# Optimization experiments

Hardware: AMD Instinct MI355X
Metric: run time of the kernel (lower is better)

The kernel has to match this reference:

```python
import jax, jax.numpy as jnp
import numpy as np

B, N, M, K = 4, 16384, 16384, 16   # batch, points, centers, neighbors
C, O, G = 64, 64, 8                # in_planes, out_planes, group


def setup_inputs() -> dict:
    key = jax.random.key(0)
    ks = jax.random.split(key, 16)
    r = lambda i, sh, s=1.0: jax.random.normal(ks[i], sh, jnp.float32) * s
    return dict(
        center_pos=r(0, (B, M, 3)),
        center_fea=r(1, (B, C, M)),
        pos=r(2, (B, N, 3)),
        fea=r(3, (B, C, N)),
        idx=jax.random.randint(ks[4], (B, M, K), 0, N, jnp.int32),
        # linear q/k/v
        Wq=r(5, (C, O), 0.05), bq=jnp.zeros((O,), jnp.float32),
        Wk=r(6, (C, O), 0.05), bk=jnp.zeros((O,), jnp.float32),
        Wv=r(7, (C, O), 0.05), bv=jnp.zeros((O,), jnp.float32),
        # center_pos_encode: conv1x1(3->O, no bias) + folded BN (scale,shift) + relu + conv1x1(O->O)
        cpe_w1=r(8, (3, O), 0.05), cpe_s=jnp.ones((O,), jnp.float32), cpe_b=jnp.zeros((O,), jnp.float32),
        cpe_w2=r(9, (O, O), 0.05), cpe_b2=jnp.zeros((O,), jnp.float32),
        # pos_encode (Conv2d 1x1 == per-point linear)
        pe_w1=r(10, (3, O), 0.05), pe_s=jnp.ones((O,), jnp.float32), pe_b=jnp.zeros((O,), jnp.float32),
        pe_w2=r(11, (O, O), 0.05), pe_b2=jnp.zeros((O,), jnp.float32),
        # weight_encode (O -> G)
        we_w1=r(12, (O, G), 0.05), we_s=jnp.ones((G,), jnp.float32), we_b=jnp.zeros((G,), jnp.float32),
        we_w2=r(13, (G, G), 0.05), we_b2=jnp.zeros((G,), jnp.float32),
    )


def _mlp2(x, w1, s, b, w2, b2):
    # conv1x1(no bias) -> inference BatchNorm folded to (scale, shift) -> ReLU -> conv1x1(+bias)
    h = jax.nn.relu(x @ w1 * s + b)
    return h @ w2 + b2


def reference(center_pos, center_fea, pos, fea, idx,
              Wq, bq, Wk, bk, Wv, bv,
              cpe_w1, cpe_s, cpe_b, cpe_w2, cpe_b2,
              pe_w1, pe_s, pe_b, pe_w2, pe_b2,
              we_w1, we_s, we_b, we_w2, we_b2):
    x_q = center_fea.transpose(0, 2, 1) @ Wq + bq        # [B,M,O]
    ft = fea.transpose(0, 2, 1)                          # [B,N,C]
    x_k = ft @ Wk + bk                                   # [B,N,O]
    x_v = ft @ Wv + bv                                   # [B,N,O]

    gather = jax.vmap(lambda a, i: a[i])                 # per-batch irregular gather
    nk = gather(x_k, idx)                                # [B,M,K,O]
    nv = gather(x_v, idx)                                # [B,M,K,O]
    npos = gather(pos, idx) - center_pos[:, :, None, :]  # [B,M,K,3] relative coords

    cpr = _mlp2(center_pos, cpe_w1, cpe_s, cpe_b, cpe_w2, cpe_b2)  # [B,M,O]
    pr = _mlp2(npos, pe_w1, pe_s, pe_b, pe_w2, pe_b2)              # [B,M,K,O]

    r_qk = nk - x_q[:, :, None, :] + cpr[:, :, None, :]  # [B,M,K,O]
    v = nv + pr                                          # [B,M,K,O]

    w = _mlp2(r_qk, we_w1, we_s, we_b, we_w2, we_b2)     # [B,M,K,G]
    w = jax.nn.softmax(w, axis=2)                        # softmax over neighbors

    v = v.reshape(B, M, K, G, O // G)
    out = jnp.einsum('bmkgi,bmkg->bmgi', v, w).reshape(B, M, O)
    return out.transpose(0, 2, 1)                        # [B,O,M]
```

## Files before the change

### kernel.cpp

```cpp
#include <hip/hip_runtime.h>
#include <hip/hip_bf16.h>

typedef unsigned short u16;
typedef __attribute__((ext_vector_type(8))) __bf16 bf8v;
typedef __attribute__((ext_vector_type(8))) _Float16 f16x8;
typedef __attribute__((ext_vector_type(2))) _Float16 h2v;
typedef __attribute__((ext_vector_type(4))) float f32x4;
typedef __attribute__((ext_vector_type(4))) unsigned uint4v;

#define B_ 4
#define N_ 16384
#define M_ 16384
#define K_ 16
#define C_ 64
#define O_ 64
#define G_ 8

__device__ __forceinline__ float bf2f(u16 x){
  union { unsigned u; float f; } v; v.u = ((unsigned)x) << 16; return v.f;
}
__device__ __forceinline__ u16 f2bf(float f){
  union { float f; unsigned u; } v; v.f = f;
  unsigned u = v.u;
  return (u16)((u + 0x7FFFu + ((u >> 16) & 1u)) >> 16);
}
__device__ __forceinline__ u16 f2h(float f){
  union { _Float16 h; u16 u; } v; v.h = (_Float16)f; return v.u;
}
__device__ __forceinline__ h2v mkh2(float a, float b){
  h2v r = {(_Float16)a, (_Float16)b}; return r;
}

__global__ __launch_bounds__(256) void pre_kernel(
    const float* __restrict__ center_pos, const float* __restrict__ center_fea,
    const float* __restrict__ pos, const float* __restrict__ fea,
    const float* __restrict__ Wq, const float* __restrict__ bq,
    const float* __restrict__ Wk, const float* __restrict__ bk,
    const float* __restrict__ Wv, const float* __restrict__ bv,
    const float* __restrict__ cpe_w1, const float* __restrict__ cpe_s, const float* __restrict__ cpe_b,
    const float* __restrict__ cpe_w2, const float* __restrict__ cpe_b2,
    const float* __restrict__ we_w1,
    u16* __restrict__ xk, u16* __restrict__ xv, float* __restrict__ qw,
    float* __restrict__ pos4, float* __restrict__ cp4)
{
  __shared__ u16 sWT[128*72];
  __shared__ u16 sA[64*72];
  __shared__ u16 sOut[64*136];
  __shared__ float sMisc[256];
  __shared__ float sCi[8];
  int tid = threadIdx.x;
  int l = tid & 63, w = tid >> 6, c = l & 15, q = l >> 4;
  int blk = blockIdx.x;

  if (blk < 256){
    int P0 = blk * 256; int b = P0 >> 14; int n00 = P0 & (N_-1);
    const float* fb = fea + (long)b*C_*N_;
    for (int e = tid; e < 8192; e += 256){
      int k = e >> 7, col = e & 127;
      float v = (col < 64) ? Wk[k*64 + col] : Wv[k*64 + (col-64)];
      sWT[col*72 + k] = f2bf(v);
    }
    if (tid < 128) sMisc[tid] = (tid < 64) ? bk[tid] : bv[tid-64];
    {
      long pg = (long)P0 + tid;
      f32x4 r = {pos[pg*3], pos[pg*3+1], pos[pg*3+2], 0.f};
      ((f32x4*)pos4)[pg] = r;
    }

    #pragma unroll 1
    for (int s = 0; s < 4; s++){
      int n0 = n00 + s*64;
      #pragma unroll
      for (int pp = 0; pp < 4; pp++){
        int k = pp*16 + (tid >> 4);
        int nf = (tid & 15)*4;
        f32x4 v = *(const f32x4*)&fb[(long)k*N_ + n0 + nf];
        sA[(nf+0)*72+k] = f2bf(v[0]); sA[(nf+1)*72+k] = f2bf(v[1]);
        sA[(nf+2)*72+k] = f2bf(v[2]); sA[(nf+3)*72+k] = f2bf(v[3]);
      }
      __syncthreads();

      bf8v af0 = *(const bf8v*)&sA[(w*16+c)*72 + q*8];
      bf8v af1 = *(const bf8v*)&sA[(w*16+c)*72 + 32 + q*8];
      f32x4 acc[8];
      #pragma unroll
      for (int t = 0; t < 8; t++){
        float bb = sMisc[16*t + c];
        f32x4 a_ = {bb, bb, bb, bb};
        bf8v b0 = *(const bf8v*)&sWT[(16*t + c)*72 + q*8];
        bf8v b1 = *(const bf8v*)&sWT[(16*t + c)*72 + 32 + q*8];
        a_ = __builtin_amdgcn_mfma_f32_16x16x32_bf16(af0, b0, a_, 0,0,0);
        a_ = __builtin_amdgcn_mfma_f32_16x16x32_bf16(af1, b1, a_, 0,0,0);
        acc[t] = a_;
      }
      #pragma unroll
      for (int t = 0; t < 8; t++)
        #pragma unroll
        for (int r = 0; r < 4; r++)
          sOut[(w*16 + q*4 + r)*136 + 16*t + c] = f2bf(acc[t][r]);
      __syncthreads();

      #pragma unroll
      for (int rep = 0; rep < 4; rep++){
        int chunk = rep*256 + tid;
        int pt = chunk >> 4, c8i = chunk & 15;
        uint4v val = *(const uint4v*)&sOut[pt*136 + c8i*8];
        int col8 = c8i*8;
        long row = (long)P0 + s*64 + pt;
        if (col8 < 64) *(uint4v*)(xk + row*64 + col8)      = val;
        else           *(uint4v*)(xv + row*64 + (col8-64)) = val;
      }
      __syncthreads();
    }
  } else {
    int P0 = (blk - 256) * 256; int b = P0 >> 14; int m00 = P0 & (M_-1);
    const float* cfb = center_fea + (long)b*C_*M_;
    float* sWe = (float*)sOut;
    float* sQ  = (float*)sOut;
    for (int e = tid; e < 512; e += 256) sWe[e] = we_w1[e];
    if (tid < 64){
      float sc = cpe_s[tid];
      sMisc[tid]     = cpe_w1[tid]*sc;
      sMisc[64+tid]  = cpe_w1[64+tid]*sc;
      sMisc[128+tid] = cpe_w1[128+tid]*sc;
      sMisc[192+tid] = cpe_b[tid];
    }
    {
      long pg = (long)P0 + tid;
      f32x4 r = {center_pos[pg*3], center_pos[pg*3+1], center_pos[pg*3+2], 0.f};
      ((f32x4*)cp4)[pg] = r;
    }
    __syncthreads();
    {
      int k = tid >> 1, g0 = (tid & 1)*4;
      const float* brow = (k < 64) ? (cpe_w2 + k*64) : (Wq + (k-64)*64);
      float sgn = (k < 64) ? 1.f : -1.f;
      float aw[4] = {0.f,0.f,0.f,0.f};
      for (int o = 0; o < 64; o++){
        float bo = brow[o]*sgn;
        #pragma unroll
        for (int gg=0; gg<4; gg++) aw[gg] += bo * sWe[o*8 + g0+gg];
      }
      #pragma unroll
      for (int gg=0; gg<4; gg++) sWT[(g0+gg)*136 + k] = f2bf(aw[gg]);
    }
    for (int e = tid; e < 2176; e += 256){
      int r = e / 136, cc = e % 136;
      if (r >= 8 || cc >= 128) sWT[e] = 0;
    }
    if (tid < 8){
      float s = 0.f;
      for (int o = 0; o < 64; o++) s += (cpe_b2[o] - bq[o]) * sWe[o*8 + tid];
      sCi[tid] = s;
    }
    __syncthreads();

    #pragma unroll 1
    for (int s = 0; s < 4; s++){
      int m0 = m00 + s*64;
      #pragma unroll
      for (int pp = 0; pp < 4; pp++){
        int k = pp*16 + (tid >> 4);
        int nf = (tid & 15)*4;
        f32x4 v = *(const f32x4*)&cfb[(long)k*M_ + m0 + nf];
        sA[(nf+0)*72+k] = f2bf(v[0]); sA[(nf+1)*72+k] = f2bf(v[1]);
        sA[(nf+2)*72+k] = f2bf(v[2]); sA[(nf+3)*72+k] = f2bf(v[3]);
      }
      long c3 = (long)(P0 + s*64 + w*16 + c)*3;
      float cp0 = center_pos[c3], cp1 = center_pos[c3+1], cp2 = center_pos[c3+2];
      __syncthreads();

      bf8v ah[2];
      #pragma unroll
      for (int ks = 0; ks < 2; ks++){
        union { bf8v v; u16 sv[8]; } ua;
        #pragma unroll
        for (int j = 0; j < 8; j++){
          int h = ks*32 + q*8 + j;
          float hv = cp0*sMisc[h] + cp1*sMisc[64+h] + cp2*sMisc[128+h] + sMisc[192+h];
          ua.sv[j] = f2bf(fmaxf(hv, 0.f));
        }
        ah[ks] = ua.v;
      }
      bf8v acf0 = *(const bf8v*)&sA[(w*16+c)*72 + q*8];
      bf8v acf1 = *(const bf8v*)&sA[(w*16+c)*72 + 32 + q*8];

      float ci = (c < 8) ? sCi[c] : 0.f;
      f32x4 aq = {ci, ci, ci, ci};
      {
        bf8v b0 = *(const bf8v*)&sWT[c*136 + q*8];
        bf8v b1 = *(const bf8v*)&sWT[c*136 + 32 + q*8];
        bf8v b2 = *(const bf8v*)&sWT[c*136 + 64 + q*8];
        bf8v b3 = *(const bf8v*)&sWT[c*136 + 96 + q*8];
        aq = __builtin_amdgcn_mfma_f32_16x16x32_bf16(ah[0], b0, aq, 0,0,0);
        aq = __builtin_amdgcn_mfma_f32_16x16x32_bf16(ah[1], b1, aq, 0,0,0);
        aq = __builtin_amdgcn_mfma_f32_16x16x32_bf16(acf0,  b2, aq, 0,0,0);
        aq = __builtin_amdgcn_mfma_f32_16x16x32_bf16(acf1,  b3, aq, 0,0,0);
      }
      __syncthreads();
      if (c < 8){
        #pragma unroll
        for (int r = 0; r < 4; r++) sQ[(w*16 + q*4 + r)*8 + c] = aq[r];
      }
      __syncthreads();
      for (int e = tid; e < 512; e += 256)
        qw[(long)(P0 + s*64)*8 + e] = sQ[e];
      __syncthreads();
    }
  }
}

__global__ __launch_bounds__(256) void attn_kernel(
    const float* __restrict__ cp4, const float* __restrict__ pos4,
    const int* __restrict__ idx,
    const float* __restrict__ pe_w1, const float* __restrict__ pe_s, const float* __restrict__ pe_b,
    const float* __restrict__ pe_w2, const float* __restrict__ pe_b2,
    const float* __restrict__ we_w1, const float* __restrict__ we_s, const float* __restrict__ we_b,
    const float* __restrict__ we_w2, const float* __restrict__ we_b2,
    const u16* __restrict__ xk, const u16* __restrict__ xv, const float* __restrict__ qw,
    float* __restrict__ out)
{
  int tid = threadIdx.x;
  __shared__ float s_w1f[192], s_pb[64], s_pb2[64], s_ww2[64];
  __shared__ float s_ws8[8], s_wb8[8], s_wb28[8];
  __shared__ f32x4 s_dyn4[1312];
  __shared__ float s_tile[32*66];

  char* dynb = (char*)s_dyn4;

  if (tid < 64){
    float sc = pe_s[tid];
    s_w1f[tid]     = pe_w1[tid]*sc;
    s_w1f[64+tid]  = pe_w1[64+tid]*sc;
    s_w1f[128+tid] = pe_w1[128+tid]*sc;
    s_pb[tid]  = pe_b[tid];
    s_pb2[tid] = pe_b2[tid];
    s_ww2[tid] = we_w2[tid];
  }
  if (tid >= 64 && tid < 72){
    int g = tid-64;
    s_ws8[g]=we_s[g]; s_wb8[g]=we_b[g]; s_wb28[g]=we_b2[g];
  }
  u16* stg = (u16*)dynb;
  #pragma unroll
  for (int pp = 0; pp < 4; pp++){
    int row = pp*16 + (tid >> 4);
    int colf = (tid & 15)*4;
    f32x4 v = *(const f32x4*)&pe_w2[row*64 + colf];
    stg[(colf+0)*72+row] = f2h(v[0]); stg[(colf+1)*72+row] = f2h(v[1]);
    stg[(colf+2)*72+row] = f2h(v[2]); stg[(colf+3)*72+row] = f2h(v[3]);
  }
  u16* stg2 = (u16*)(dynb + 9216);
  for (int e = tid; e < 512; e += 256){
    int k = e >> 3, cc = e & 7;
    stg2[cc*72 + k] = f2bf(we_w1[e]);
  }
  for (int e = tid; e < 576; e += 256) stg2[576 + e] = 0;
  __syncthreads();

  int w = tid >> 6, l = tid & 63, c = l & 15, q = l >> 4, c8 = c & 7, qb = l & 48;

  f16x8 pw2f[4][2];
  bf8v ww1f[2];
  f16x8 w2B, hz8;
  #pragma unroll
  for (int t = 0; t < 4; t++){
    pw2f[t][0] = *(const f16x8*)&stg[(t*16+c)*72 + q*8];
    pw2f[t][1] = *(const f16x8*)&stg[(t*16+c)*72 + 32 + q*8];
  }
  ww1f[0] = *(const bf8v*)&stg2[c*72 + q*8];
  ww1f[1] = *(const bf8v*)&stg2[c*72 + 32 + q*8];
  {
    union { f16x8 v; u16 s[8]; } uu;
    #pragma unroll
    for (int j = 0; j < 8; j++)
      uu.s[j] = (q == 0 && c < 8) ? f2h(s_ww2[j*8 + c]) : (u16)0;
    w2B = uu.v;
    #pragma unroll
    for (int j = 0; j < 8; j++) uu.s[j] = 0;
    hz8 = uu.v;
  }
  h2v cw0[2][4], cw1[2][4], cw2[2][4], cb[2][4];
  #pragma unroll
  for (int ks = 0; ks < 2; ks++)
    #pragma unroll
    for (int jj = 0; jj < 4; jj++){
      int o = ks*32 + q*8 + jj*2;
      cw0[ks][jj] = mkh2(s_w1f[o],     s_w1f[o+1]);
      cw1[ks][jj] = mkh2(s_w1f[64+o],  s_w1f[65+o]);
      cw2[ks][jj] = mkh2(s_w1f[128+o], s_w1f[129+o]);
      cb [ks][jj] = mkh2(s_pb[o],      s_pb[o+1]);
    }
  float ws_c = s_ws8[c8], wb_c = s_wb8[c8], wb2_c = s_wb28[c8];
  float pb2l = s_pb2[l];
  h2v hz2 = {(_Float16)0.f, (_Float16)0.f};
  __syncthreads();

  float* sv  = (float*)(dynb + w*5248);
  float* swt = (float*)(dynb + w*5248 + 4352);
  u16*  sh   = (u16*) (dynb + w*5248 + 4992);

  int pbase = blockIdx.x * 32;
  int b = pbase >> 14;
  const u16* xkb = xk + (long)b * N_ * 64;
  const u16* xvb = xv + (long)b * N_ * 64;
  const f32x4* pos4b = ((const f32x4*)pos4) + (long)b * N_;
  int ch = c >> 3;
  int gl = l >> 3;

  int pb0 = pbase + w*8;
  const int*   idxl = idx + (long)pb0*16 + c;
  const float* qwl  = qw  + (long)pb0*8 + c8;
  const f32x4* cp4l = ((const f32x4*)cp4) + pb0;

  int iv = idxl[0];
  float qpv = qwl[0];
  f32x4 cpv = cp4l[0];
  f32x4 ppv = pos4b[iv];
  const u16* kr0 = xkb + (size_t)iv*64;
  bf8v ka0 = *(const bf8v*)(kr0 + q*8);
  bf8v ka1 = *(const bf8v*)(kr0 + 32 + q*8);
  const u16* vr0 = xvb + (size_t)iv*64;
  uint4v va0 = *(const uint4v*)(vr0 + q*8);
  uint4v va1 = *(const uint4v*)(vr0 + 32 + q*8);

  #pragma unroll 1
  for (int i = 0; i < 8; i++){
    int ni = (i < 7) ? i+1 : i;
    int iv_n = idxl[ni*16];
    float qpv_n = qwl[ni*8];
    f32x4 cpn = cp4l[ni];
    f32x4 ppn = pos4b[iv_n];
    const u16* krn = xkb + (size_t)iv_n*64;
    bf8v kan0 = *(const bf8v*)(krn + q*8);
    bf8v kan1 = *(const bf8v*)(krn + 32 + q*8);
    const u16* vrn = xvb + (size_t)iv_n*64;
    uint4v van0 = *(const uint4v*)(vrn + q*8);
    uint4v van1 = *(const uint4v*)(vrn + 32 + q*8);

    {
      f32x4 f0, f1, f2, f3;
      #pragma unroll
      for (int jj = 0; jj < 2; jj++){
        unsigned u0 = va0[jj*2], u1 = va0[jj*2+1];
        f0[jj*2]   = bf2f((u16)u0); f0[jj*2+1] = bf2f((u16)(u0>>16));
        f1[jj*2]   = bf2f((u16)u1); f1[jj*2+1] = bf2f((u16)(u1>>16));
      }
      unsigned a0 = va0[0], a1 = va0[1], a2 = va0[2], a3 = va0[3];
      f32x4 lo0 = {bf2f((u16)a0), bf2f((u16)(a0>>16)), bf2f((u16)a1), bf2f((u16)(a1>>16))};
      f32x4 hi0 = {bf2f((u16)a2), bf2f((u16)(a2>>16)), bf2f((u16)a3), bf2f((u16)(a3>>16))};
      unsigned b0 = va1[0], b1 = va1[1], b2 = va1[2], b3 = va1[3];
      f32x4 lo1 = {bf2f((u16)b0), bf2f((u16)(b0>>16)), bf2f((u16)b1), bf2f((u16)(b1>>16))};
      f32x4 hi1 = {bf2f((u16)b2), bf2f((u16)(b2>>16)), bf2f((u16)b3), bf2f((u16)(b3>>16))};
      f32x4* d0 = (f32x4*)&sv[c*68 + q*8];
      d0[0] = lo0; d0[1] = hi0;
      f32x4* d1 = (f32x4*)&sv[c*68 + 32 + q*8];
      d1[0] = lo1; d1[1] = hi1;
    }

    float np0 = ppv[0] - cpv[0], np1 = ppv[1] - cpv[1], np2 = ppv[2] - cpv[2];
    h2v np0h = {(_Float16)np0, (_Float16)np0};
    h2v np1h = {(_Float16)np1, (_Float16)np1};
    h2v np2h = {(_Float16)np2, (_Float16)np2};
    f16x8 h1f[2];
    #pragma unroll
    for (int ks = 0; ks < 2; ks++){
      union { f16x8 v; h2v p[4]; } hu;
      #pragma unroll
      for (int jj = 0; jj < 4; jj++){
        h2v a = cb[ks][jj];
        a = np0h*cw0[ks][jj] + a;
        a = np1h*cw1[ks][jj] + a;
        a = np2h*cw2[ks][jj] + a;
        hu.p[jj] = __builtin_elementwise_max(a, hz2);
      }
      h1f[ks] = hu.v;
    }

    f32x4 h2a = {qpv, qpv, qpv, qpv};
    h2a = __builtin_amdgcn_mfma_f32_16x16x32_bf16(ka0, ww1f[0], h2a, 0,0,0);
    h2a = __builtin_amdgcn_mfma_f32_16x16x32_bf16(ka1, ww1f[1], h2a, 0,0,0);

    if (c < 8){
      #pragma unroll
      for (int r = 0; r < 4; r++)
        sh[(q*4+r)*8 + c] = f2h(fmaxf(h2a[r]*ws_c + wb_c, 0.f));
    }
    f16x8 hrow = *(const f16x8*)&sh[c*8];
    f16x8 ahf = (q == 0) ? hrow : hz8;

    f32x4 wlv = {wb2_c, wb2_c, wb2_c, wb2_c};
    wlv = __builtin_amdgcn_mfma_f32_16x16x32_f16(ahf, w2B, wlv, 0,0,0);

    float e0 = exp2f(wlv[0]*1.44269504f);
    float e1 = exp2f(wlv[1]*1.44269504f);
    float e2 = exp2f(wlv[2]*1.44269504f);
    float e3 = exp2f(wlv[3]*1.44269504f);
    float sm = e0+e1+e2+e3;
    sm += __shfl_xor(sm, 16, 64);
    sm += __shfl_xor(sm, 32, 64);
    float rn = 1.0f / sm;
    if (c < 8){
      f32x4 ev = {e0*rn, e1*rn, e2*rn, e3*rn};
      *(f32x4*)&swt[c*20 + q*4] = ev;
    }

    float ov[4];
    #pragma unroll
    for (int t = 0; t < 4; t++){
      f32x4 z = {0.f,0.f,0.f,0.f};
      z = __builtin_amdgcn_mfma_f32_16x16x32_f16(h1f[0], pw2f[t][0], z, 0,0,0);
      z = __builtin_amdgcn_mfma_f32_16x16x32_f16(h1f[1], pw2f[t][1], z, 0,0,0);
      f32x4 wv = *(const f32x4*)&swt[(t*2+ch)*20 + q*4];
      ov[t] = z[0]*wv[0] + z[1]*wv[1] + z[2]*wv[2] + z[3]*wv[3];
    }
    #pragma unroll
    for (int t = 0; t < 4; t++){
      ov[t] += __shfl_xor(ov[t], 16, 64);
      ov[t] += __shfl_xor(ov[t], 32, 64);
    }
    float ovsel = ov[0];
    ovsel = (q==1) ? ov[1] : ovsel;
    ovsel = (q==2) ? ov[2] : ovsel;
    ovsel = (q==3) ? ov[3] : ovsel;

    float vacc = 0.f;
    {
      const f32x4* wr4 = (const f32x4*)&swt[gl*20];
      const float* svl = &sv[l];
      #pragma unroll
      for (int k4 = 0; k4 < 4; k4++){
        f32x4 wv = wr4[k4];
        vacc += svl[(4*k4+0)*68]*wv[0];
        vacc += svl[(4*k4+1)*68]*wv[1];
        vacc += svl[(4*k4+2)*68]*wv[2];
        vacc += svl[(4*k4+3)*68]*wv[3];
      }
    }

    s_tile[(w*8+i)*66 + l] = ovsel + vacc + pb2l;

    iv = iv_n; qpv = qpv_n; cpv = cpn; ppv = ppn;
    ka0 = kan0; ka1 = kan1; va0 = van0; va1 = van1;
  }
  __syncthreads();

  int o0 = tid >> 5, pt = tid & 31;
  int m0 = pbase & (M_-1);
  long outb = ((long)b*64) * M_ + m0 + pt;
  #pragma unroll
  for (int ii = 0; ii < 8; ii++){
    int o = o0*8 + ii;
    out[outb + (long)o*M_] = s_tile[pt*66 + o];
  }
}

extern "C" void kernel_launch(void* const* d_in, const int* in_sizes, int n_in,
                              void* d_out, int out_size, void* d_ws, size_t ws_size,
                              hipStream_t stream) {
  const float* center_pos = (const float*)d_in[0];
  const float* center_fea = (const float*)d_in[1];
  const float* pos        = (const float*)d_in[2];
  const float* fea        = (const float*)d_in[3];
  const int*   idx        = (const int*)d_in[4];
  const float* Wq = (const float*)d_in[5];   const float* bq = (const float*)d_in[6];
  const float* Wk = (const float*)d_in[7];   const float* bk = (const float*)d_in[8];
  const float* Wv = (const float*)d_in[9];   const float* bv = (const float*)d_in[10];
  const float* cpe_w1 = (const float*)d_in[11]; const float* cpe_s = (const float*)d_in[12];
  const float* cpe_b  = (const float*)d_in[13]; const float* cpe_w2 = (const float*)d_in[14];
  const float* cpe_b2 = (const float*)d_in[15];
  const float* pe_w1 = (const float*)d_in[16]; const float* pe_s = (const float*)d_in[17];
  const float* pe_b  = (const float*)d_in[18]; const float* pe_w2 = (const float*)d_in[19];
  const float* pe_b2 = (const float*)d_in[20];
  const float* we_w1 = (const float*)d_in[21]; const float* we_s = (const float*)d_in[22];
  const float* we_b  = (const float*)d_in[23]; const float* we_w2 = (const float*)d_in[24];
  const float* we_b2 = (const float*)d_in[25];

  const size_t SZ = (size_t)B_*N_*64;
  u16* xk = (u16*)d_ws;
  u16* xv = xk + SZ;
  float* qwp = (float*)(xv + SZ);
  float* pos4p = qwp + (size_t)B_*M_*8;
  float* cp4p  = pos4p + (size_t)B_*N_*4;
  float* outp = (float*)d_out;

  hipLaunchKernelGGL(pre_kernel, dim3(512), dim3(256), 0, stream,
      center_pos, center_fea, pos, fea, Wq, bq, Wk, bk, Wv, bv,
      cpe_w1, cpe_s, cpe_b, cpe_w2, cpe_b2, we_w1,
      xk, xv, qwp, pos4p, cp4p);
  hipLaunchKernelGGL(attn_kernel, dim3(2048), dim3(256), 0, stream,
      cp4p, pos4p, idx, pe_w1, pe_s, pe_b, pe_w2, pe_b2,
      we_w1, we_s, we_b, we_w2, we_b2, xk, xv, qwp, outp);
}
```

Measured before the change: 207.7 us.

## Shrink attention LDS footprint with bf16/fp16 staging and interleave pre blocks

The attention kernel now stages gathered V rows in LDS as raw bf16 instead of unpacked fp32, and keeps the output tile as fp16. This cuts shared memory per block so more blocks fit per CU, and the launch bound now requests 6 waves per EU. It also swaps exp2f for the hardware exp2 builtin. The pre kernel interleaves key/value and query blocks by parity instead of splitting them into two halves. Storing the output tile as fp16 adds rounding error to the final result.

```diff
diff --git a/kernel.cpp b/kernel.cpp
--- a/kernel.cpp
+++ b/kernel.cpp
@@ -26,6 +26,9 @@
 }
 __device__ __forceinline__ u16 f2h(float f){
   union { _Float16 h; u16 u; } v; v.h = (_Float16)f; return v.u;
+}
+__device__ __forceinline__ float h2f(u16 x){
+  union { u16 u; _Float16 h; } v; v.u = x; return (float)v.h;
 }
 __device__ __forceinline__ h2v mkh2(float a, float b){
   h2v r = {(_Float16)a, (_Float16)b}; return r;
@@ -51,9 +54,10 @@
   int tid = threadIdx.x;
   int l = tid & 63, w = tid >> 6, c = l & 15, q = l >> 4;
   int blk = blockIdx.x;
-
-  if (blk < 256){
-    int P0 = blk * 256; int b = P0 >> 14; int n00 = P0 & (N_-1);
+  int half = blk >> 1;
+
+  if ((blk & 1) == 0){
+    int P0 = half * 256; int b = P0 >> 14; int n00 = P0 & (N_-1);
     const float* fb = fea + (long)b*C_*N_;
     for (int e = tid; e < 8192; e += 256){
       int k = e >> 7, col = e & 127;
@@ -113,7 +117,7 @@
       __syncthreads();
     }
   } else {
-    int P0 = (blk - 256) * 256; int b = P0 >> 14; int m00 = P0 & (M_-1);
+    int P0 = half * 256; int b = P0 >> 14; int m00 = P0 & (M_-1);
     const float* cfb = center_fea + (long)b*C_*M_;
     float* sWe = (float*)sOut;
     float* sQ  = (float*)sOut;
@@ -210,7 +214,7 @@
   }
 }
 
-__global__ __launch_bounds__(256) void attn_kernel(
+__global__ __launch_bounds__(256, 6) void attn_kernel(
     const float* __restrict__ cp4, const float* __restrict__ pos4,
     const int* __restrict__ idx,
     const float* __restrict__ pe_w1, const float* __restrict__ pe_s, const float* __restrict__ pe_b,
@@ -223,8 +227,8 @@
   int tid = threadIdx.x;
   __shared__ float s_w1f[192], s_pb[64], s_pb2[64], s_ww2[64];
   __shared__ float s_ws8[8], s_wb8[8], s_wb28[8];
-  __shared__ f32x4 s_dyn4[1312];
-  __shared__ float s_tile[32*66];
+  __shared__ f32x4 s_dyn4[800];
+  __shared__ u16  s_tile[32*66];
 
   char* dynb = (char*)s_dyn4;
 
@@ -258,7 +262,7 @@
   for (int e = tid; e < 576; e += 256) stg2[576 + e] = 0;
   __syncthreads();
 
-  int w = tid >> 6, l = tid & 63, c = l & 15, q = l >> 4, c8 = c & 7, qb = l & 48;
+  int w = tid >> 6, l = tid & 63, c = l & 15, q = l >> 4, c8 = c & 7;
 
   f16x8 pw2f[4][2];
   bf8v ww1f[2];
@@ -296,9 +300,9 @@
   h2v hz2 = {(_Float16)0.f, (_Float16)0.f};
   __syncthreads();
 
-  float* sv  = (float*)(dynb + w*5248);
-  float* swt = (float*)(dynb + w*5248 + 4352);
-  u16*  sh   = (u16*) (dynb + w*5248 + 4992);
+  u16*  sv  = (u16*) (dynb + w*3200);
+  float* swt = (float*)(dynb + w*3200 + 2304);
+  u16*  sh   = (u16*) (dynb + w*3200 + 2944);
 
   int pbase = blockIdx.x * 32;
   int b = pbase >> 14;
@@ -338,25 +342,8 @@
     uint4v van0 = *(const uint4v*)(vrn + q*8);
     uint4v van1 = *(const uint4v*)(vrn + 32 + q*8);
 
-    {
-      f32x4 f0, f1, f2, f3;
-      #pragma unroll
-      for (int jj = 0; jj < 2; jj++){
-        unsigned u0 = va0[jj*2], u1 = va0[jj*2+1];
-        f0[jj*2]   = bf2f((u16)u0); f0[jj*2+1] = bf2f((u16)(u0>>16));
-        f1[jj*2]   = bf2f((u16)u1); f1[jj*2+1] = bf2f((u16)(u1>>16));
-      }
-      unsigned a0 = va0[0], a1 = va0[1], a2 = va0[2], a3 = va0[3];
-      f32x4 lo0 = {bf2f((u16)a0), bf2f((u16)(a0>>16)), bf2f((u16)a1), bf2f((u16)(a1>>16))};
-      f32x4 hi0 = {bf2f((u16)a2), bf2f((u16)(a2>>16)), bf2f((u16)a3), bf2f((u16)(a3>>16))};
-      unsigned b0 = va1[0], b1 = va1[1], b2 = va1[2], b3 = va1[3];
-      f32x4 lo1 = {bf2f((u16)b0), bf2f((u16)(b0>>16)), bf2f((u16)b1), bf2f((u16)(b1>>16))};
-      f32x4 hi1 = {bf2f((u16)b2), bf2f((u16)(b2>>16)), bf2f((u16)b3), bf2f((u16)(b3>>16))};
-      f32x4* d0 = (f32x4*)&sv[c*68 + q*8];
-      d0[0] = lo0; d0[1] = hi0;
-      f32x4* d1 = (f32x4*)&sv[c*68 + 32 + q*8];
-      d1[0] = lo1; d1[1] = hi1;
-    }
+    *(uint4v*)&sv[c*72 + q*8]      = va0;
+    *(uint4v*)&sv[c*72 + 32 + q*8] = va1;
 
     float np0 = ppv[0] - cpv[0], np1 = ppv[1] - cpv[1], np2 = ppv[2] - cpv[2];
     h2v np0h = {(_Float16)np0, (_Float16)np0};
@@ -392,10 +379,10 @@
     f32x4 wlv = {wb2_c, wb2_c, wb2_c, wb2_c};
     wlv = __builtin_amdgcn_mfma_f32_16x16x32_f16(ahf, w2B, wlv, 0,0,0);
 
-    float e0 = exp2f(wlv[0]*1.44269504f);
-    float e1 = exp2f(wlv[1]*1.44269504f);
-    float e2 = exp2f(wlv[2]*1.44269504f);
-    float e3 = exp2f(wlv[3]*1.44269504f);
+    float e0 = __builtin_amdgcn_exp2f(wlv[0]*1.44269504f);
+    float e1 = __builtin_amdgcn_exp2f(wlv[1]*1.44269504f);
+    float e2 = __builtin_amdgcn_exp2f(wlv[2]*1.44269504f);
+    float e3 = __builtin_amdgcn_exp2f(wlv[3]*1.44269504f);
     float sm = e0+e1+e2+e3;
     sm += __shfl_xor(sm, 16, 64);
     sm += __shfl_xor(sm, 32, 64);
@@ -427,18 +414,17 @@
     float vacc = 0.f;
     {
       const f32x4* wr4 = (const f32x4*)&swt[gl*20];
-      const float* svl = &sv[l];
       #pragma unroll
       for (int k4 = 0; k4 < 4; k4++){
         f32x4 wv = wr4[k4];
-        vacc += svl[(4*k4+0)*68]*wv[0];
-        vacc += svl[(4*k4+1)*68]*wv[1];
-        vacc += svl[(4*k4+2)*68]*wv[2];
-        vacc += svl[(4*k4+3)*68]*wv[3];
-      }
-    }
-
-    s_tile[(w*8+i)*66 + l] = ovsel + vacc + pb2l;
+        vacc += bf2f(sv[(4*k4+0)*72 + l])*wv[0];
+        vacc += bf2f(sv[(4*k4+1)*72 + l])*wv[1];
+        vacc += bf2f(sv[(4*k4+2)*72 + l])*wv[2];
+        vacc += bf2f(sv[(4*k4+3)*72 + l])*wv[3];
+      }
+    }
+
+    s_tile[(w*8+i)*66 + l] = f2h(ovsel + vacc + pb2l);
 
     iv = iv_n; qpv = qpv_n; cpv = cpn; ppv = ppn;
     ka0 = kan0; ka1 = kan1; va0 = van0; va1 = van1;
@@ -451,7 +437,7 @@
   #pragma unroll
   for (int ii = 0; ii < 8; ii++){
     int o = o0*8 + ii;
-    out[outb + (long)o*M_] = s_tile[pt*66 + o];
+    out[outb + (long)o*M_] = h2f(s_tile[pt*66 + o]);
   }
 }
 
```

Result: slower. 415.2 us (+99.9%).
